# Kernel optimization log

Hardware: AMD Instinct MI355X
Metric: run time of the kernel (lower is better)

## Reference

```python
import jax, jax.numpy as jnp
import numpy as np

GRID_SIZE = 5
SPLINE_ORDER = 3
EPS = 1e-5


def make_grid(in_features):
    # efficient-kan: grid_range=[-1,1], points from -order..grid_size+order
    h = 2.0 / GRID_SIZE
    g = jnp.arange(-SPLINE_ORDER, GRID_SIZE + SPLINE_ORDER + 1, dtype=jnp.float32) * h - 1.0
    return jnp.tile(g[None, :], (in_features, 1))  # [in, grid_size + 2*order + 1]


def b_splines(x, grid):
    # x: [B, in], grid: [in, G] -> bases: [B, in, grid_size + order]
    xg = x[:, :, None]
    bases = ((xg >= grid[:, :-1]) & (xg < grid[:, 1:])).astype(x.dtype)
    for k in range(1, SPLINE_ORDER + 1):
        left = (xg - grid[:, : -(k + 1)]) / (grid[:, k:-1] - grid[:, : -(k + 1)])
        right = (grid[:, k + 1:] - xg) / (grid[:, k + 1:] - grid[:, 1:-k])
        bases = left * bases[:, :, :-1] + right * bases[:, :, 1:]
    return bases


def kan_linear(x, grid, base_w, spline_w, spline_scaler):
    # base path: silu(x) @ base_w.T ; spline path: bsplines(x) contracted with scaled spline weight
    base_out = jnp.einsum('bi,oi->bo', jax.nn.silu(x), base_w)
    bases = b_splines(x, grid)  # [B, in, C]
    sw = spline_w * spline_scaler[:, :, None]  # [out, in, C]
    spline_out = jnp.einsum('bic,oic->bo', bases, sw)
    return base_out + spline_out


def layer_norm(x, w, b):
    mu = jnp.mean(x, axis=-1, keepdims=True)
    var = jnp.mean(jnp.square(x - mu), axis=-1, keepdims=True)
    return (x - mu) * jax.lax.rsqrt(var + EPS) * w + b


def setup_inputs() -> dict:
    key = jax.random.key(0)
    ks = jax.random.split(key, 8)
    B, F, H, E = 65536, 32, 64, 64
    OUT = E * F  # 2048
    C = GRID_SIZE + SPLINE_ORDER  # 8 coeffs per edge
    x = jax.random.normal(ks[0], (B, F), dtype=jnp.float32)
    return {
        'x': x,
        'ln_w': jnp.ones((F,), jnp.float32),
        'ln_b': jnp.zeros((F,), jnp.float32),
        'bw1': jax.random.normal(ks[1], (H, F), jnp.float32) * 0.1,
        'sw1': jax.random.normal(ks[2], (H, F, C), jnp.float32) * 0.1,
        'ss1': jax.random.normal(ks[3], (H, F), jnp.float32) * 0.1 + 1.0,
        'bw2': jax.random.normal(ks[4], (OUT, H), jnp.float32) * 0.1,
        'sw2': jax.random.normal(ks[5], (OUT, H, C), jnp.float32) * 0.1,
        'ss2': jax.random.normal(ks[6], (OUT, H), jnp.float32) * 0.1 + 1.0,
        'grid1': make_grid(F),
        'grid2': make_grid(H),
    }


def reference(x, ln_w, ln_b, bw1, sw1, ss1, bw2, sw2, ss2, grid1, grid2):
    h = layer_norm(x, ln_w, ln_b)
    h = kan_linear(h, grid1, bw1, sw1, ss1)   # [B, 64]
    out = kan_linear(h, grid2, bw2, sw2, ss2)  # [B, 2048]
    return out
```

## Files before the change

kernel.cpp:

```cpp
#include <hip/hip_runtime.h>
#include <stdint.h>

#define BATCH   65536
#define FIN     32
#define HID     64
#define NOUT    2048
#define NC      8
#define NF      9
#define K1      288
#define K2      576

#define BM8     128
#define BN8     128
#define BK8     32
#define KT8     18

typedef __bf16 bf16x8 __attribute__((ext_vector_type(8)));
typedef float f32x4 __attribute__((ext_vector_type(4)));

__device__ __forceinline__ uint16_t f2bf(float f) {
    uint32_t u = __builtin_bit_cast(uint32_t, f);
    uint32_t r = (u + 0x7fffu + ((u >> 16) & 1u)) >> 16;
    return (uint16_t)r;
}
__device__ __forceinline__ float silu_f(float v) {
    return v / (1.f + __expf(-v));
}

__device__ __forceinline__ void bspline8u(float xv, float out[8]) {
    float s = (xv + 2.2f) * 2.5f;
    int c = (int)floorf(s);
    float gc = (float)(c - 3) * 0.4f - 1.0f;
    float u = (xv - gc) * 2.5f;
    float u1 = 1.f - u;
    float uu = u * u, u3 = uu * u;
    float w0 = u1 * u1 * u1 * (1.f / 6.f);
    float w1 = (3.f * u3 - 6.f * uu + 4.f) * (1.f / 6.f);
    float w2 = (-3.f * u3 + 3.f * uu + 3.f * u + 1.f) * (1.f / 6.f);
    float w3 = u3 * (1.f / 6.f);
#pragma unroll
    for (int t = 0; t < 8; t++) {
        int d = c - t;
        out[t] = (d == 0) ? w3 : (d == 1) ? w2 : (d == 2) ? w1 : (d == 3) ? w0 : 0.f;
    }
}

__global__ void pack_w1(const float* __restrict__ bw1, const float* __restrict__ sw1,
                        const float* __restrict__ ss1, uint16_t* __restrict__ w1L) {
    int idx = blockIdx.x * 256 + threadIdx.x;
    if (idx >= 64 * K1) return;
    int o = idx / K1, k = idx % K1;
    int i = k / 9, j = k % 9;
    float v = (j == 0) ? bw1[o * FIN + i]
                       : sw1[(o * FIN + i) * NC + (j - 1)] * ss1[o * FIN + i];
    w1L[idx] = f2bf(v);
}

__global__ void pack_w2(const float* __restrict__ bw2, const float* __restrict__ sw2,
                        const float* __restrict__ ss2, uint16_t* __restrict__ w2p) {
    int idx = blockIdx.x * 256 + threadIdx.x;
    if (idx >= NOUT * K2) return;
    int n = idx / K2, k = idx % K2;
    int j = k >> 6, i = k & 63;
    float v = (j == 0) ? bw2[n * HID + i]
                       : sw2[(n * HID + i) * NC + (j - 1)] * ss2[n * HID + i];
    w2p[idx] = f2bf(v);
}

#define FBR    64
#define A1LD   296
#define S2LD   584
__global__ __launch_bounds__(256) void featurize(
    const float* __restrict__ x, const float* __restrict__ lnw, const float* __restrict__ lnb,
    const uint16_t* __restrict__ w1L, uint16_t* __restrict__ a2) {

    __shared__ __align__(16) char fsm[75776];
    uint16_t* w1s = (uint16_t*)fsm;
    uint16_t* a1s = (uint16_t*)(fsm + 37888);
    uint16_t* s2  = (uint16_t*)fsm;

    const int tid = threadIdx.x;
    const int wv = tid >> 6, lane = tid & 63;
    const int rowBase = blockIdx.x * FBR;

#pragma unroll
    for (int t = 0; t < 9; ++t) {
        int idx = t * 256 + tid;
        int o = idx / 36, cc = idx % 36;
        uint4 v = *(const uint4*)(w1L + idx * 8);
        *(uint4*)&w1s[o * A1LD + cc * 8] = v;
    }

    const int prow = tid >> 2, pq = tid & 3;
    const float* xp = x + (size_t)(rowBase + prow) * FIN + pq * 8;
    float xv[8];
    *(float4*)&xv[0] = ((const float4*)xp)[0];
    *(float4*)&xv[4] = ((const float4*)xp)[1];
    float s = 0.f, s2v = 0.f;
#pragma unroll
    for (int j = 0; j < 8; j++) { s += xv[j]; s2v += xv[j] * xv[j]; }
    s += __shfl_xor(s, 1);  s2v += __shfl_xor(s2v, 1);
    s += __shfl_xor(s, 2);  s2v += __shfl_xor(s2v, 2);
    const float mu = s * (1.f / 32.f);
    const float var = s2v * (1.f / 32.f) - mu * mu;
    const float rstd = rsqrtf(var + 1e-5f);

    float wl[8], bl[8];
    *(float4*)&wl[0] = ((const float4*)(lnw + pq * 8))[0];
    *(float4*)&wl[4] = ((const float4*)(lnw + pq * 8))[1];
    *(float4*)&bl[0] = ((const float4*)(lnb + pq * 8))[0];
    *(float4*)&bl[4] = ((const float4*)(lnb + pq * 8))[1];

    __align__(16) uint16_t tmp[72];
#pragma unroll
    for (int ii = 0; ii < 8; ii++) {
        float xn = (xv[ii] - mu) * rstd * wl[ii] + bl[ii];
        tmp[ii * 9] = f2bf(silu_f(xn));
        float bs[8];
        bspline8u(xn, bs);
#pragma unroll
        for (int j = 0; j < 8; j++) tmp[ii * 9 + 1 + j] = f2bf(bs[j]);
    }
    {
        uint16_t* dst = &a1s[prow * A1LD + pq * 72];
#pragma unroll
        for (int q = 0; q < 9; q++) *(uint4*)(dst + q * 8) = *(const uint4*)&tmp[q * 8];
    }
    __syncthreads();

    f32x4 acc[4];
#pragma unroll
    for (int n = 0; n < 4; n++) acc[n] = (f32x4){0.f, 0.f, 0.f, 0.f};
    const int arow = wv * 16 + (lane & 15);
    const int koff = (lane >> 4) * 8;
#pragma unroll
    for (int ks = 0; ks < 9; ++ks) {
        bf16x8 af = *(const bf16x8*)&a1s[arow * A1LD + ks * 32 + koff];
#pragma unroll
        for (int n = 0; n < 4; n++) {
            bf16x8 bv = *(const bf16x8*)&w1s[(n * 16 + (lane & 15)) * A1LD + ks * 32 + koff];
            acc[n] = __builtin_amdgcn_mfma_f32_16x16x32_bf16(af, bv, acc[n], 0, 0, 0);
        }
    }
    __syncthreads();

    const int r0 = wv * 16 + ((lane >> 4) << 2);
    const int cb = lane & 15;
#pragma unroll
    for (int n = 0; n < 4; n++)
#pragma unroll
        for (int r = 0; r < 4; r++) {
            float h = acc[n][r];
            float o9[9];
            o9[0] = silu_f(h);
            bspline8u(h, &o9[1]);
            uint16_t* op = &s2[(size_t)(r0 + r) * S2LD + n * 16 + cb];
#pragma unroll
            for (int j = 0; j < 9; j++) op[j * 64] = f2bf(o9[j]);
        }
    __syncthreads();

#pragma unroll
    for (int q = 0; q < 18; ++q) {
        int g = q * 256 + tid;
        int row = g / 72, c = g % 72;
        uint4 v = *(const uint4*)&s2[row * S2LD + c * 8];
        *(uint4*)(a2 + (size_t)(rowBase + row) * K2 + c * 8) = v;
    }
}

__device__ __forceinline__ void gload16(const uint16_t* g, const uint16_t* l) {
    __builtin_amdgcn_global_load_lds(
        (const __attribute__((address_space(1))) void*)g,
        (__attribute__((address_space(3))) void*)l, 16, 0, 0);
}

__global__ __launch_bounds__(256) void gemm2_kernel(const uint16_t* __restrict__ A,
                                                    const uint16_t* __restrict__ Bt,
                                                    float* __restrict__ C) {
    __shared__ __align__(16) uint16_t As[2][BM8 * BK8];
    __shared__ __align__(16) uint16_t Bs[2][BM8 * BK8];

    const int tid = threadIdx.x;
    const int wv = tid >> 6, lane = tid & 63;
    const int wr = wv >> 1, wc = wv & 1;

    const uint32_t bid = blockIdx.x;
    const uint32_t wk = (bid & 7u) * 1024u + (bid >> 3);
    const uint32_t ntile = wk & 15u, mtile = wk >> 4;

    const int srow = tid >> 2;
    const int scol = (((tid & 3) ^ (srow & 3)) << 3);
    const uint16_t* gA = A  + (size_t)(mtile * BM8 + srow) * K2 + scol;
    const uint16_t* gB = Bt + (size_t)(ntile * BN8 + srow) * K2 + scol;

#define ST8(b, t) do { \
    gload16(gA + (t) * BK8,                    &As[b][wv * 512]); \
    gload16(gA + (size_t)64 * K2 + (t) * BK8,  &As[b][2048 + wv * 512]); \
    gload16(gB + (t) * BK8,                    &Bs[b][wv * 512]); \
    gload16(gB + (size_t)64 * K2 + (t) * BK8,  &Bs[b][2048 + wv * 512]); } while (0)

    const int fswz = (((lane >> 4) ^ (lane & 3)) << 3);
    const int aoff = (wr * 64 + (lane & 15)) * BK8 + fswz;
    const int boff = (wc * 64 + (lane & 15)) * BK8 + fswz;

    f32x4 acc[4][4];
#pragma unroll
    for (int m = 0; m < 4; m++)
#pragma unroll
        for (int n = 0; n < 4; n++) acc[m][n] = (f32x4){0.f, 0.f, 0.f, 0.f};

    ST8(0, 0);
    __syncthreads();

#pragma unroll 2
    for (int t = 0; t < KT8; ++t) {
        const int b = t & 1;
        if (t + 1 < KT8) ST8(b ^ 1, t + 1);

        bf16x8 af[4], bv[4];
#pragma unroll
        for (int m = 0; m < 4; ++m) af[m] = *(const bf16x8*)&As[b][aoff + m * 16 * BK8];
#pragma unroll
        for (int n = 0; n < 4; ++n) bv[n] = *(const bf16x8*)&Bs[b][boff + n * 16 * BK8];
#pragma unroll
        for (int m = 0; m < 4; ++m)
#pragma unroll
            for (int n = 0; n < 4; ++n)
                acc[m][n] = __builtin_amdgcn_mfma_f32_16x16x32_bf16(af[m], bv[n], acc[m][n], 0, 0, 0);

        __syncthreads();
    }
#undef ST8

    const int crow0 = (int)mtile * BM8 + wr * 64 + ((lane >> 4) << 2);
    const int ccol0 = (int)ntile * BN8 + wc * 64 + (lane & 15);
#pragma unroll
    for (int m = 0; m < 4; ++m)
#pragma unroll
        for (int n = 0; n < 4; ++n) {
            float* cp = C + (size_t)(crow0 + m * 16) * NOUT + ccol0 + n * 16;
#pragma unroll
            for (int r = 0; r < 4; ++r) cp[(size_t)r * NOUT] = acc[m][n][r];
        }
}

extern "C" void kernel_launch(void* const* d_in, const int* in_sizes, int n_in,
                              void* d_out, int out_size, void* d_ws, size_t ws_size,
                              hipStream_t stream) {
    const float* x    = (const float*)d_in[0];
    const float* lnw  = (const float*)d_in[1];
    const float* lnb  = (const float*)d_in[2];
    const float* bw1  = (const float*)d_in[3];
    const float* sw1  = (const float*)d_in[4];
    const float* ss1  = (const float*)d_in[5];
    const float* bw2  = (const float*)d_in[6];
    const float* sw2  = (const float*)d_in[7];
    const float* ss2  = (const float*)d_in[8];

    char* ws = (char*)d_ws;
    uint16_t* w1L = (uint16_t*)ws;
    uint16_t* w2p = (uint16_t*)(ws + 65536);
    uint16_t* a2  = (uint16_t*)(ws + 65536 + 2359296);
    float* out = (float*)d_out;

    pack_w1<<<dim3(72), dim3(256), 0, stream>>>(bw1, sw1, ss1, w1L);
    pack_w2<<<dim3((NOUT * K2 + 255) / 256), dim3(256), 0, stream>>>(bw2, sw2, ss2, w2p);
    featurize<<<dim3(BATCH / FBR), dim3(256), 0, stream>>>(x, lnw, lnb, w1L, a2);
    gemm2_kernel<<<dim3((BATCH / BM8) * (NOUT / BN8)), dim3(256), 0, stream>>>(a2, w2p, out);
}
```

Before: 341.4 us.

## Widen GEMM K-tile to 64 and loop blocks over four M-tiles

The second GEMM now stages 64-wide K slices, which halves the number of barrier iterations, and uses an 8-way XOR swizzle to match. Each block walks four consecutive 128-row M tiles for one N tile, prefetching the next tile's first slice across the tile boundary, which cuts the grid size by four. The B tile is reloaded for every M tile, so no reuse is gained from that, but launch and prologue overhead are amortised and the pipeline stays full between tiles. LDS per block doubles to 64KB, which may reduce occupancy, and fewer blocks may leave compute units idle at the tail.

```diff
diff --git a/kernel.cpp b/kernel.cpp
--- a/kernel.cpp
+++ b/kernel.cpp
@@ -10,10 +10,9 @@
 #define K1      288
 #define K2      576
 
-#define BM8     128
-#define BN8     128
-#define BK8     32
-#define KT8     18
+#define BKW     64
+#define KT9     9
+#define MT      4
 
 typedef __bf16 bf16x8 __attribute__((ext_vector_type(8)));
 typedef float f32x4 __attribute__((ext_vector_type(4)));
@@ -178,71 +177,84 @@
 __global__ __launch_bounds__(256) void gemm2_kernel(const uint16_t* __restrict__ A,
                                                     const uint16_t* __restrict__ Bt,
                                                     float* __restrict__ C) {
-    __shared__ __align__(16) uint16_t As[2][BM8 * BK8];
-    __shared__ __align__(16) uint16_t Bs[2][BM8 * BK8];
+    __shared__ __align__(16) uint16_t As[2][128 * BKW];
+    __shared__ __align__(16) uint16_t Bs[2][128 * BKW];
 
     const int tid = threadIdx.x;
     const int wv = tid >> 6, lane = tid & 63;
     const int wr = wv >> 1, wc = wv & 1;
 
     const uint32_t bid = blockIdx.x;
-    const uint32_t wk = (bid & 7u) * 1024u + (bid >> 3);
-    const uint32_t ntile = wk & 15u, mtile = wk >> 4;
-
-    const int srow = tid >> 2;
-    const int scol = (((tid & 3) ^ (srow & 3)) << 3);
-    const uint16_t* gA = A  + (size_t)(mtile * BM8 + srow) * K2 + scol;
-    const uint16_t* gB = Bt + (size_t)(ntile * BN8 + srow) * K2 + scol;
-
-#define ST8(b, t) do { \
-    gload16(gA + (t) * BK8,                    &As[b][wv * 512]); \
-    gload16(gA + (size_t)64 * K2 + (t) * BK8,  &As[b][2048 + wv * 512]); \
-    gload16(gB + (t) * BK8,                    &Bs[b][wv * 512]); \
-    gload16(gB + (size_t)64 * K2 + (t) * BK8,  &Bs[b][2048 + wv * 512]); } while (0)
-
-    const int fswz = (((lane >> 4) ^ (lane & 3)) << 3);
-    const int aoff = (wr * 64 + (lane & 15)) * BK8 + fswz;
-    const int boff = (wc * 64 + (lane & 15)) * BK8 + fswz;
+    const uint32_t wk = (bid & 7u) * 256u + (bid >> 3);
+    const uint32_t ntile = wk & 15u;
+    const uint32_t mgrp  = wk >> 4;
+
+    const int srow = tid >> 3;
+    const int scol = (((tid & 7) ^ (srow & 7)) << 3);
+    const uint16_t* gA = A  + ((size_t)mgrp * 512 + srow) * K2 + scol;
+    const uint16_t* gB = Bt + ((size_t)ntile * 128 + srow) * K2 + scol;
+
+#define STA(b, mt, t) do { _Pragma("unroll") \
+    for (int r = 0; r < 4; ++r) \
+        gload16(gA + (size_t)((mt) * 128 + r * 32) * K2 + (t) * BKW, \
+                &As[b][r * 2048 + wv * 512]); } while (0)
+#define STB(b, t) do { _Pragma("unroll") \
+    for (int r = 0; r < 4; ++r) \
+        gload16(gB + (size_t)(r * 32) * K2 + (t) * BKW, \
+                &Bs[b][r * 2048 + wv * 512]); } while (0)
+
+    const int swz0 = (((lane >> 4)      ) ^ (lane & 7)) << 3;
+    const int swz1 = (((lane >> 4) | 4  ) ^ (lane & 7)) << 3;
+    const int abase = (wr * 64 + (lane & 15)) * BKW;
+    const int bbase = (wc * 64 + (lane & 15)) * BKW;
 
     f32x4 acc[4][4];
-#pragma unroll
-    for (int m = 0; m < 4; m++)
-#pragma unroll
-        for (int n = 0; n < 4; n++) acc[m][n] = (f32x4){0.f, 0.f, 0.f, 0.f};
-
-    ST8(0, 0);
-    __syncthreads();
-
-#pragma unroll 2
-    for (int t = 0; t < KT8; ++t) {
-        const int b = t & 1;
-        if (t + 1 < KT8) ST8(b ^ 1, t + 1);
-
-        bf16x8 af[4], bv[4];
-#pragma unroll
-        for (int m = 0; m < 4; ++m) af[m] = *(const bf16x8*)&As[b][aoff + m * 16 * BK8];
-#pragma unroll
-        for (int n = 0; n < 4; ++n) bv[n] = *(const bf16x8*)&Bs[b][boff + n * 16 * BK8];
+
+    STA(0, 0, 0); STB(0, 0);
+    __syncthreads();
+
+    for (int mt = 0; mt < MT; ++mt) {
+#pragma unroll
+        for (int m = 0; m < 4; m++)
+#pragma unroll
+            for (int n = 0; n < 4; n++) acc[m][n] = (f32x4){0.f, 0.f, 0.f, 0.f};
+
+#pragma unroll
+        for (int t = 0; t < KT9; ++t) {
+            const int b = (mt * KT9 + t) & 1;
+            if (t < KT9 - 1)      { STA(b ^ 1, mt, t + 1); STB(b ^ 1, t + 1); }
+            else if (mt + 1 < MT) { STA(b ^ 1, mt + 1, 0); STB(b ^ 1, 0); }
+
+#pragma unroll
+            for (int ks = 0; ks < 2; ++ks) {
+                const int swz = ks ? swz1 : swz0;
+                bf16x8 af[4], bv[4];
+#pragma unroll
+                for (int m = 0; m < 4; ++m) af[m] = *(const bf16x8*)&As[b][abase + m * 16 * BKW + swz];
+#pragma unroll
+                for (int n = 0; n < 4; ++n) bv[n] = *(const bf16x8*)&Bs[b][bbase + n * 16 * BKW + swz];
+#pragma unroll
+                for (int m = 0; m < 4; ++m)
+#pragma unroll
+                    for (int n = 0; n < 4; ++n)
+                        acc[m][n] = __builtin_amdgcn_mfma_f32_16x16x32_bf16(af[m], bv[n], acc[m][n], 0, 0, 0);
+            }
+            __syncthreads();
+        }
+
+        const int crow0 = (int)mgrp * 512 + mt * 128 + wr * 64 + ((lane >> 4) << 2);
+        const int ccol0 = (int)ntile * 128 + wc * 64 + (lane & 15);
 #pragma unroll
         for (int m = 0; m < 4; ++m)
 #pragma unroll
-            for (int n = 0; n < 4; ++n)
-                acc[m][n] = __builtin_amdgcn_mfma_f32_16x16x32_bf16(af[m], bv[n], acc[m][n], 0, 0, 0);
-
-        __syncthreads();
-    }
-#undef ST8
-
-    const int crow0 = (int)mtile * BM8 + wr * 64 + ((lane >> 4) << 2);
-    const int ccol0 = (int)ntile * BN8 + wc * 64 + (lane & 15);
-#pragma unroll
-    for (int m = 0; m < 4; ++m)
-#pragma unroll
-        for (int n = 0; n < 4; ++n) {
-            float* cp = C + (size_t)(crow0 + m * 16) * NOUT + ccol0 + n * 16;
-#pragma unroll
-            for (int r = 0; r < 4; ++r) cp[(size_t)r * NOUT] = acc[m][n][r];
-        }
+            for (int n = 0; n < 4; ++n) {
+                float* cp = C + (size_t)(crow0 + m * 16) * NOUT + ccol0 + n * 16;
+#pragma unroll
+                for (int r = 0; r < 4; ++r) cp[(size_t)r * NOUT] = acc[m][n][r];
+            }
+    }
+#undef STA
+#undef STB
 }
 
 extern "C" void kernel_launch(void* const* d_in, const int* in_sizes, int n_in,
@@ -267,5 +279,5 @@
     pack_w1<<<dim3(72), dim3(256), 0, stream>>>(bw1, sw1, ss1, w1L);
     pack_w2<<<dim3((NOUT * K2 + 255) / 256), dim3(256), 0, stream>>>(bw2, sw2, ss2, w2p);
     featurize<<<dim3(BATCH / FBR), dim3(256), 0, stream>>>(x, lnw, lnb, w1L, a2);
-    gemm2_kernel<<<dim3((BATCH / BM8) * (NOUT / BN8)), dim3(256), 0, stream>>>(a2, w2p, out);
-}
+    gemm2_kernel<<<dim3((BATCH / (128 * MT)) * (NOUT / 128)), dim3(256), 0, stream>>>(a2, w2p, out);
+}
```

Measured after the change: 371.3 us. 8.7% more time.

## Fuse featurization with second GEMM, keeping activations in LDS

Applied to the files above, without the earlier changes.

Merges the featurize kernel and the second-layer GEMM into one kernel. Each 512-thread block computes 128 rows of layer-2 features into LDS in a k-major layout and then runs a 32x32x16 MFMA GEMM over all 2048 outputs, streaming the repacked weights straight from global memory into registers. This drops the round trip of the bf16 activation matrix through HBM and one kernel launch. In exchange, each block re-reads the whole weight matrix (likely served from L2), uses 144KB of LDS with launch bounds of (512,2), and has no LDS staging for B.

```diff
diff --git a/kernel.cpp b/kernel.cpp
--- a/kernel.cpp
+++ b/kernel.cpp
@@ -10,13 +10,9 @@
 #define K1      288
 #define K2      576
 
-#define BM8     128
-#define BN8     128
-#define BK8     32
-#define KT8     18
-
 typedef __bf16 bf16x8 __attribute__((ext_vector_type(8)));
-typedef float f32x4 __attribute__((ext_vector_type(4)));
+typedef float f32x4  __attribute__((ext_vector_type(4)));
+typedef float f32x16 __attribute__((ext_vector_type(16)));
 
 __device__ __forceinline__ uint16_t f2bf(float f) {
     uint32_t u = __builtin_bit_cast(uint32_t, f);
@@ -56,38 +52,37 @@
     w1L[idx] = f2bf(v);
 }
 
-__global__ void pack_w2(const float* __restrict__ bw2, const float* __restrict__ sw2,
-                        const float* __restrict__ ss2, uint16_t* __restrict__ w2p) {
+__global__ void pack_w2km(const float* __restrict__ bw2, const float* __restrict__ sw2,
+                          const float* __restrict__ ss2, uint16_t* __restrict__ w2km) {
     int idx = blockIdx.x * 256 + threadIdx.x;
-    if (idx >= NOUT * K2) return;
-    int n = idx / K2, k = idx % K2;
+    int slot = idx >> 14;
+    int n = (idx >> 3) & 2047;
+    int e = idx & 7;
+    int k = slot * 8 + e;
     int j = k >> 6, i = k & 63;
     float v = (j == 0) ? bw2[n * HID + i]
                        : sw2[(n * HID + i) * NC + (j - 1)] * ss2[n * HID + i];
-    w2p[idx] = f2bf(v);
-}
-
-#define FBR    64
+    w2km[idx] = f2bf(v);
+}
+
 #define A1LD   296
-#define S2LD   584
-__global__ __launch_bounds__(256) void featurize(
+__global__ __launch_bounds__(512, 2) void kan_fused(
     const float* __restrict__ x, const float* __restrict__ lnw, const float* __restrict__ lnb,
-    const uint16_t* __restrict__ w1L, uint16_t* __restrict__ a2) {
-
-    __shared__ __align__(16) char fsm[75776];
+    const uint16_t* __restrict__ w1L, const uint16_t* __restrict__ w2km,
+    float* __restrict__ C) {
+
+    __shared__ __align__(16) char fsm[147456];
     uint16_t* w1s = (uint16_t*)fsm;
     uint16_t* a1s = (uint16_t*)(fsm + 37888);
-    uint16_t* s2  = (uint16_t*)fsm;
+    const char* a2kb = fsm;
 
     const int tid = threadIdx.x;
     const int wv = tid >> 6, lane = tid & 63;
-    const int rowBase = blockIdx.x * FBR;
-
-#pragma unroll
-    for (int t = 0; t < 9; ++t) {
-        int idx = t * 256 + tid;
-        int o = idx / 36, cc = idx % 36;
-        uint4 v = *(const uint4*)(w1L + idx * 8);
+    const int rowBase = blockIdx.x * 128;
+
+    for (int i = tid; i < 2304; i += 512) {
+        int o = i / 36, cc = i % 36;
+        uint4 v = *(const uint4*)(w1L + i * 8);
         *(uint4*)&w1s[o * A1LD + cc * 8] = v;
     }
 
@@ -128,9 +123,9 @@
     }
     __syncthreads();
 
-    f32x4 acc[4];
-#pragma unroll
-    for (int n = 0; n < 4; n++) acc[n] = (f32x4){0.f, 0.f, 0.f, 0.f};
+    f32x4 acc1[4];
+#pragma unroll
+    for (int n = 0; n < 4; n++) acc1[n] = (f32x4){0.f, 0.f, 0.f, 0.f};
     const int arow = wv * 16 + (lane & 15);
     const int koff = (lane >> 4) * 8;
 #pragma unroll
@@ -139,110 +134,86 @@
 #pragma unroll
         for (int n = 0; n < 4; n++) {
             bf16x8 bv = *(const bf16x8*)&w1s[(n * 16 + (lane & 15)) * A1LD + ks * 32 + koff];
-            acc[n] = __builtin_amdgcn_mfma_f32_16x16x32_bf16(af, bv, acc[n], 0, 0, 0);
+            acc1[n] = __builtin_amdgcn_mfma_f32_16x16x32_bf16(af, bv, acc1[n], 0, 0, 0);
         }
     }
     __syncthreads();
 
-    const int r0 = wv * 16 + ((lane >> 4) << 2);
-    const int cb = lane & 15;
-#pragma unroll
-    for (int n = 0; n < 4; n++)
-#pragma unroll
-        for (int r = 0; r < 4; r++) {
-            float h = acc[n][r];
-            float o9[9];
-            o9[0] = silu_f(h);
-            bspline8u(h, &o9[1]);
-            uint16_t* op = &s2[(size_t)(r0 + r) * S2LD + n * 16 + cb];
-#pragma unroll
-            for (int j = 0; j < 9; j++) op[j * 64] = f2bf(o9[j]);
+    {
+        const int r0 = wv * 16 + ((lane >> 4) << 2);
+        const int cb = lane & 15;
+        uint16_t* a2w = (uint16_t*)fsm;
+#pragma unroll
+        for (int n = 0; n < 4; n++)
+#pragma unroll
+            for (int r = 0; r < 4; r++) {
+                float h = acc1[n][r];
+                float o9[9];
+                o9[0] = silu_f(h);
+                bspline8u(h, &o9[1]);
+#pragma unroll
+                for (int j = 0; j < 9; j++) {
+                    int c = n * 16 + cb + j * 64;
+                    a2w[(c >> 3) * 1024 + (r0 + r) * 8 + (c & 7)] = f2bf(o9[j]);
+                }
+            }
+    }
+    __syncthreads();
+
+    const int r5 = lane & 31, kg = lane >> 5;
+    const char* aB = a2kb + kg * 2048 + r5 * 16;
+    const char* bB = (const char*)w2km + kg * 32768 + (wv * 256 + r5) * 16;
+
+#define LOADB(G, g, nfo) do { _Pragma("unroll") \
+    for (int ss = 0; ss < 4; ++ss) \
+        G[ss] = *(const bf16x8*)(bB + (nfo) + (size_t)((g) * 4 + ss) * 65536); } while (0)
+
+#define COMP4(G, g) do { _Pragma("unroll") \
+    for (int ss = 0; ss < 4; ++ss) { \
+        const char* ap = aB + (size_t)((g) * 4 + ss) * 4096; \
+        bf16x8 am0 = *(const bf16x8*)(ap); \
+        bf16x8 am1 = *(const bf16x8*)(ap + 512); \
+        bf16x8 am2 = *(const bf16x8*)(ap + 1024); \
+        bf16x8 am3 = *(const bf16x8*)(ap + 1536); \
+        acc[0] = __builtin_amdgcn_mfma_f32_32x32x16_bf16(am0, G[ss], acc[0], 0, 0, 0); \
+        acc[1] = __builtin_amdgcn_mfma_f32_32x32x16_bf16(am1, G[ss], acc[1], 0, 0, 0); \
+        acc[2] = __builtin_amdgcn_mfma_f32_32x32x16_bf16(am2, G[ss], acc[2], 0, 0, 0); \
+        acc[3] = __builtin_amdgcn_mfma_f32_32x32x16_bf16(am3, G[ss], acc[3], 0, 0, 0); \
+    } } while (0)
+
+#pragma unroll
+    for (int nf = 0; nf < 8; ++nf) {
+        const int nfo = nf * 512;
+        f32x16 acc[4];
+#pragma unroll
+        for (int m = 0; m < 4; m++)
+#pragma unroll
+            for (int r = 0; r < 16; r++) acc[m][r] = 0.f;
+
+        bf16x8 B0[4], B1[4], B2[4];
+        LOADB(B0, 0, nfo); LOADB(B1, 1, nfo);
+        LOADB(B2, 2, nfo); COMP4(B0, 0);
+        LOADB(B0, 3, nfo); COMP4(B1, 1);
+        LOADB(B1, 4, nfo); COMP4(B2, 2);
+        LOADB(B2, 5, nfo); COMP4(B0, 3);
+        LOADB(B0, 6, nfo); COMP4(B1, 4);
+        LOADB(B1, 7, nfo); COMP4(B2, 5);
+        LOADB(B2, 8, nfo); COMP4(B0, 6);
+        COMP4(B1, 7);
+        COMP4(B2, 8);
+
+        const int colA = wv * 256 + nf * 32 + r5;
+        const int crow = rowBase + 4 * kg;
+#pragma unroll
+        for (int m = 0; m < 4; ++m) {
+            float* cp = C + (size_t)(crow + m * 32) * NOUT + colA;
+#pragma unroll
+            for (int r = 0; r < 16; ++r)
+                cp[(size_t)((r & 3) + 8 * (r >> 2)) * NOUT] = acc[m][r];
         }
-    __syncthreads();
-
-#pragma unroll
-    for (int q = 0; q < 18; ++q) {
-        int g = q * 256 + tid;
-        int row = g / 72, c = g % 72;
-        uint4 v = *(const uint4*)&s2[row * S2LD + c * 8];
-        *(uint4*)(a2 + (size_t)(rowBase + row) * K2 + c * 8) = v;
-    }
-}
-
-__device__ __forceinline__ void gload16(const uint16_t* g, const uint16_t* l) {
-    __builtin_amdgcn_global_load_lds(
-        (const __attribute__((address_space(1))) void*)g,
-        (__attribute__((address_space(3))) void*)l, 16, 0, 0);
-}
-
-__global__ __launch_bounds__(256) void gemm2_kernel(const uint16_t* __restrict__ A,
-                                                    const uint16_t* __restrict__ Bt,
-                                                    float* __restrict__ C) {
-    __shared__ __align__(16) uint16_t As[2][BM8 * BK8];
-    __shared__ __align__(16) uint16_t Bs[2][BM8 * BK8];
-
-    const int tid = threadIdx.x;
-    const int wv = tid >> 6, lane = tid & 63;
-    const int wr = wv >> 1, wc = wv & 1;
-
-    const uint32_t bid = blockIdx.x;
-    const uint32_t wk = (bid & 7u) * 1024u + (bid >> 3);
-    const uint32_t ntile = wk & 15u, mtile = wk >> 4;
-
-    const int srow = tid >> 2;
-    const int scol = (((tid & 3) ^ (srow & 3)) << 3);
-    const uint16_t* gA = A  + (size_t)(mtile * BM8 + srow) * K2 + scol;
-    const uint16_t* gB = Bt + (size_t)(ntile * BN8 + srow) * K2 + scol;
-
-#define ST8(b, t) do { \
-    gload16(gA + (t) * BK8,                    &As[b][wv * 512]); \
-    gload16(gA + (size_t)64 * K2 + (t) * BK8,  &As[b][2048 + wv * 512]); \
-    gload16(gB + (t) * BK8,                    &Bs[b][wv * 512]); \
-    gload16(gB + (size_t)64 * K2 + (t) * BK8,  &Bs[b][2048 + wv * 512]); } while (0)
-
-    const int fswz = (((lane >> 4) ^ (lane & 3)) << 3);
-    const int aoff = (wr * 64 + (lane & 15)) * BK8 + fswz;
-    const int boff = (wc * 64 + (lane & 15)) * BK8 + fswz;
-
-    f32x4 acc[4][4];
-#pragma unroll
-    for (int m = 0; m < 4; m++)
-#pragma unroll
-        for (int n = 0; n < 4; n++) acc[m][n] = (f32x4){0.f, 0.f, 0.f, 0.f};
-
-    ST8(0, 0);
-    __syncthreads();
-
-#pragma unroll 2
-    for (int t = 0; t < KT8; ++t) {
-        const int b = t & 1;
-        if (t + 1 < KT8) ST8(b ^ 1, t + 1);
-
-        bf16x8 af[4], bv[4];
-#pragma unroll
-        for (int m = 0; m < 4; ++m) af[m] = *(const bf16x8*)&As[b][aoff + m * 16 * BK8];
-#pragma unroll
-        for (int n = 0; n < 4; ++n) bv[n] = *(const bf16x8*)&Bs[b][boff + n * 16 * BK8];
-#pragma unroll
-        for (int m = 0; m < 4; ++m)
-#pragma unroll
-            for (int n = 0; n < 4; ++n)
-                acc[m][n] = __builtin_amdgcn_mfma_f32_16x16x32_bf16(af[m], bv[n], acc[m][n], 0, 0, 0);
-
-        __syncthreads();
-    }
-#undef ST8
-
-    const int crow0 = (int)mtile * BM8 + wr * 64 + ((lane >> 4) << 2);
-    const int ccol0 = (int)ntile * BN8 + wc * 64 + (lane & 15);
-#pragma unroll
-    for (int m = 0; m < 4; ++m)
-#pragma unroll
-        for (int n = 0; n < 4; ++n) {
-            float* cp = C + (size_t)(crow0 + m * 16) * NOUT + ccol0 + n * 16;
-#pragma unroll
-            for (int r = 0; r < 4; ++r) cp[(size_t)r * NOUT] = acc[m][n][r];
-        }
+    }
+#undef LOADB
+#undef COMP4
 }
 
 extern "C" void kernel_launch(void* const* d_in, const int* in_sizes, int n_in,
@@ -259,13 +230,11 @@
     const float* ss2  = (const float*)d_in[8];
 
     char* ws = (char*)d_ws;
-    uint16_t* w1L = (uint16_t*)ws;
-    uint16_t* w2p = (uint16_t*)(ws + 65536);
-    uint16_t* a2  = (uint16_t*)(ws + 65536 + 2359296);
+    uint16_t* w1L  = (uint16_t*)ws;
+    uint16_t* w2km = (uint16_t*)(ws + 65536);
     float* out = (float*)d_out;
 
     pack_w1<<<dim3(72), dim3(256), 0, stream>>>(bw1, sw1, ss1, w1L);
-    pack_w2<<<dim3((NOUT * K2 + 255) / 256), dim3(256), 0, stream>>>(bw2, sw2, ss2, w2p);
-    featurize<<<dim3(BATCH / FBR), dim3(256), 0, stream>>>(x, lnw, lnb, w1L, a2);
-    gemm2_kernel<<<dim3((BATCH / BM8) * (NOUT / BN8)), dim3(256), 0, stream>>>(a2, w2p, out);
-}
+    pack_w2km<<<dim3(4608), dim3(256), 0, stream>>>(bw2, sw2, ss2, w2km);
+    kan_fused<<<dim3(BATCH / 128), dim3(512), 0, stream>>>(x, lnw, lnb, w1L, w2km, out);
+}
```

Measured after the change: 514.0 us. 50.5% more time.
